# Optimization experiments

Hardware: AMD Instinct MI355X
Metric: run time of the kernel (lower is better)

Reference implementation:

```python
import jax, jax.numpy as jnp
import numpy as np

EPS = 1e-5

def binarize(x):
    # det Binarize: sign with zeros mapped to +1
    return jnp.where(x >= 0, 1.0, -1.0).astype(x.dtype)

def conv3x3(x, w, stride=1):
    return jax.lax.conv_general_dilated(
        x, w, window_strides=(stride, stride), padding=((1, 1), (1, 1)),
        dimension_numbers=('NCHW', 'OIHW', 'NCHW'))

def batchnorm_train(x, gamma, beta):
    # training-mode BN: biased batch stats over (N, H, W)
    mean = jnp.mean(x, axis=(0, 2, 3), keepdims=True)
    var = jnp.mean(jnp.square(x - mean), axis=(0, 2, 3), keepdims=True)
    xn = (x - mean) * jax.lax.rsqrt(var + EPS)
    return xn * gamma[None, :, None, None] + beta[None, :, None, None]

def setup_inputs() -> dict:
    key = jax.random.key(0)
    k1, k2, k3 = jax.random.split(key, 3)
    C = 256
    return {
        'x': jax.random.normal(k1, (64, C, 28, 28), dtype=jnp.float32),
        'w1': jax.random.normal(k2, (C, C, 3, 3), dtype=jnp.float32) * 0.05,
        'w2': jax.random.normal(k3, (C, C, 3, 3), dtype=jnp.float32) * 0.05,
        'gamma1': jnp.ones((C,), jnp.float32),
        'beta1': jnp.zeros((C,), jnp.float32),
        'gamma2': jnp.ones((C,), jnp.float32),
        'beta2': jnp.zeros((C,), jnp.float32),
    }

def reference(x, w1, w2, gamma1, beta1, gamma2, beta2):
    residual = x
    # conv1: binarized activations and weights, 3x3 pad=1 stride=1
    out = conv3x3(binarize(x), binarize(w1))
    out = batchnorm_train(out, gamma1, beta1)
    out = jnp.clip(out, -1.0, 1.0)  # Hardtanh
    # conv2
    out = conv3x3(binarize(out), binarize(w2))
    out = out + residual
    # do_bntan
    out = batchnorm_train(out, gamma2, beta2)
    out = jnp.clip(out, -1.0, 1.0)
    return out
```

## Files before the change

kernel.cpp:

```cpp
#include <hip/hip_runtime.h>
#include <stdint.h>

typedef int v4i __attribute__((ext_vector_type(4)));

constexpr int C     = 256;
constexpr int H     = 28, W = 28;
constexpr int HW    = H * W;
constexpr int NB    = 64;
constexpr int GP    = NB * HW;
constexpr int CNT   = GP;
constexpr int TOTAL = NB * C * HW;
constexpr int MT    = 112;
constexpr int NBLK  = GP / MT;
constexpr int LROWS = 176;
constexpr int ZROW  = LROWS * 16;
constexpr int GPB   = GP / 256;

__device__ __forceinline__ void pack_x_item(int local, int t, const float* __restrict__ x,
                                            v4i* __restrict__ xb, double* __restrict__ stats) {
    const int ch = local / GPB;
    const int gp = (local % GPB) * 256 + t;
    if (ch == 0 && gp < 1024) stats[gp] = 0.0;
    const int n = gp / HW, p = gp % HW;
    const float* base = x + (size_t)n * C * HW + p + (size_t)(ch * 16) * HW;
    int b0 = 0, b1 = 0, b2 = 0, b3 = 0;
#pragma unroll
    for (int e = 0; e < 16; ++e) {
        float v = base[(size_t)e * HW];
        int b = (v < 0.f) ? 0xFF : 0x01;
        int sh = (e & 3) * 8;
        if (e < 4) b0 |= b << sh; else if (e < 8) b1 |= b << sh;
        else if (e < 12) b2 |= b << sh; else b3 |= b << sh;
    }
    v4i o; o.x = b0; o.y = b1; o.z = b2; o.w = b3;
    xb[(size_t)ch * GP + gp] = o;
}

__device__ __forceinline__ void finalize_coefs(int t, const double* __restrict__ sum,
                                               const double* __restrict__ sumsq,
                                               const float* __restrict__ gamma,
                                               const float* __restrict__ beta,
                                               float* __restrict__ s_scale,
                                               float* __restrict__ s_shift) {
    double mean = sum[t] / (double)CNT;
    double var  = sumsq[t] / (double)CNT - mean * mean;
    double inv  = 1.0 / sqrt(var + 1e-5);
    s_scale[t] = (float)inv * gamma[t];
    s_shift[t] = beta[t] - (float)(mean * inv) * gamma[t];
}

__global__ void pack_all_kernel(const float* __restrict__ pw1, const float* __restrict__ pw2,
                                const float* __restrict__ x,
                                v4i* __restrict__ wbf1, v4i* __restrict__ wbf2,
                                v4i* __restrict__ xb, double* __restrict__ stats) {
    __shared__ signed char sgn[36864];
    const int t = threadIdx.x;
    const int bid = blockIdx.x;
    if (bid < 32) {
        const int g = bid & 15;
        const float* w = (bid >> 4) ? pw2 : pw1;
        v4i* dst       = (bid >> 4) ? wbf2 : wbf1;
        const float4* wg = (const float4*)(w + (size_t)g * 16 * 2304);
        int* sg4 = (int*)sgn;
        for (int pass = 0; pass < 36; ++pass) {
            const int m4 = pass * 256 + t;
            float4 v = wg[m4];
            int pk = (v.x < 0.f ? 0xFF : 0x01)
                   | ((v.y < 0.f ? 0xFF : 0x01) << 8)
                   | ((v.z < 0.f ? 0xFF : 0x01) << 16)
                   | ((v.w < 0.f ? 0xFF : 0x01) << 24);
            sg4[m4] = pk;
        }
        __syncthreads();
        const int l = t & 63, kb = t >> 6;
        const int colb = (l & 15) * 2304;
        const int cib  = kb * 64 + (l >> 4) * 16;
        for (int tp = 0; tp < 9; ++tp) {
            int b0 = 0, b1 = 0, b2 = 0, b3 = 0;
#pragma unroll
            for (int e = 0; e < 16; ++e) {
                int b = (int)(unsigned char)sgn[colb + (cib + e) * 9 + tp];
                int sh = (e & 3) * 8;
                if (e < 4) b0 |= b << sh; else if (e < 8) b1 |= b << sh;
                else if (e < 12) b2 |= b << sh; else b3 |= b << sh;
            }
            v4i o; o.x = b0; o.y = b1; o.z = b2; o.w = b3;
            dst[((tp * 4 + kb) * 16 + g) * 64 + l] = o;
        }
    } else {
        pack_x_item(bid - 32, t, x, xb, stats);
    }
}

__global__ void bn_signpack_kernel(const short* __restrict__ y,
                                   const double* __restrict__ sum,
                                   const double* __restrict__ sumsq,
                                   const float* __restrict__ gamma,
                                   const float* __restrict__ beta,
                                   v4i* __restrict__ xb) {
    __shared__ float s_scale[C], s_shift[C];
    const int t = threadIdx.x;
    finalize_coefs(t, sum, sumsq, gamma, beta, s_scale, s_shift);
    __syncthreads();
    const int local = blockIdx.x;
    const int ch = local / GPB;
    const int gp = (local % GPB) * 256 + t;
    const int n = gp / HW, p = gp % HW;
    const short* base = y + (size_t)n * C * HW + p + (size_t)(ch * 16) * HW;
    int b0 = 0, b1 = 0, b2 = 0, b3 = 0;
#pragma unroll
    for (int e = 0; e < 16; ++e) {
        const int c = ch * 16 + e;
        float z = (float)base[(size_t)e * HW] * s_scale[c] + s_shift[c];
        int b = (z < 0.f) ? 0xFF : 0x01;
        int sh = (e & 3) * 8;
        if (e < 4) b0 |= b << sh; else if (e < 8) b1 |= b << sh;
        else if (e < 12) b2 |= b << sh; else b3 |= b << sh;
    }
    v4i o; o.x = b0; o.y = b1; o.z = b2; o.w = b3;
    xb[(size_t)ch * GP + gp] = o;
}


#define ACCD(m) v4i c##m##_0={0,0,0,0}, c##m##_1={0,0,0,0}, \
                    c##m##_2={0,0,0,0}, c##m##_3={0,0,0,0};
#define ACC_DECL ACCD(0) ACCD(1) ACCD(2) ACCD(3) ACCD(4) ACCD(5) ACCD(6)

#define MFMA(a,b,c) c = __builtin_amdgcn_mfma_i32_16x16x64_i8(a, b, c, 0, 0, 0);

#define B_LOADQ(P, idx) { const v4i* bp = wbf + (idx); \
    P##0 = bp[0]; P##1 = bp[64]; P##2 = bp[128]; P##3 = bp[192]; }

#define ARD(P, m, cb) P##m = xl[R##m + ((cb) ^ S##m)];
#define ARDALL(P, cb) ARD(P,0,cb) ARD(P,1,cb) ARD(P,2,cb) ARD(P,3,cb) \
                      ARD(P,4,cb) ARD(P,5,cb) ARD(P,6,cb)

#define MFMAG(A,B,g) MFMA(A##0,B##g,c0_##g) MFMA(A##1,B##g,c1_##g) MFMA(A##2,B##g,c2_##g) \
                     MFMA(A##3,B##g,c3_##g) MFMA(A##4,B##g,c4_##g) MFMA(A##5,B##g,c5_##g) \
                     MFMA(A##6,B##g,c6_##g)
#define MFMA_C(A,B) __builtin_amdgcn_s_setprio(1); \
    MFMAG(A,B,0) MFMAG(A,B,1) MFMAG(A,B,2) MFMAG(A,B,3) \
    __builtin_amdgcn_s_setprio(0);

#define TV1(m) { const bool mk = ((unsigned)(cm##m + dc) < 28u) && \
                                 ((unsigned)(rm##m + dr) < 28u); \
    R##m = mk ? (lrb + 16 * (m)) * 16 : ZROW; S##m = mk ? sm : 0; }
#define TAPVARS(TPX) { const int dr = (TPX)/3 - 1, dc = (TPX)%3 - 1; \
    const int lrb = 32 + llo + dr * W + dc; const int sm = lrb & 15; \
    TV1(0) TV1(1) TV1(2) TV1(3) TV1(4) TV1(5) TV1(6) }

#define PMV(m) const int gx##m = gp0 + (m)*16 + llo; \
    const int pmv##m = gx##m % HW; \
    const int rm##m = pmv##m / W, cm##m = pmv##m % W;

#define EPIV(m,g) { \
    const int gpv = gp0 + (m)*16 + lhi*4; \
    const int nn = gpv / HW; const int pp = gpv - nn*HW; \
    const size_t base = (size_t)nn*(C*HW) + (size_t)(wn*64+(g)*16+llo)*HW + pp; \
    const v4i cc = c##m##_##g; \
    if constexpr (HAS_RES) { \
        const float4 r = *(const float4*)(residual + base); \
        float4 o; o.x = (float)cc.x + r.x; o.y = (float)cc.y + r.y; \
        o.z = (float)cc.z + r.z; o.w = (float)cc.w + r.w; \
        *(float4*)((float*)yout + base) = o; \
        sy##g += o.x + o.y + o.z + o.w; \
        sq##g += o.x*o.x + o.y*o.y + o.z*o.z + o.w*o.w; \
    } else { \
        int2 o; o.x = (cc.x & 0xFFFF) | (cc.y << 16); \
        o.y = (cc.z & 0xFFFF) | (cc.w << 16); \
        *(int2*)((short*)yout + base) = o; \
        const float fx = (float)cc.x, fy = (float)cc.y, fz = (float)cc.z, fw = (float)cc.w; \
        sy##g += fx + fy + fz + fw; \
        sq##g += fx*fx + fy*fy + fz*fz + fw*fw; \
    } }
#define EPIM(m) EPIV(m,0) EPIV(m,1) EPIV(m,2) EPIV(m,3)

#define REDN(g) { float s1 = sy##g, s2 = sq##g; \
    s1 += __shfl_down(s1, 32); s1 += __shfl_down(s1, 16); \
    s2 += __shfl_down(s2, 32); s2 += __shfl_down(s2, 16); \
    if (l < 16) { const int co = wn*64 + (g)*16 + l; \
        atomicAdd(&sum[co], (double)s1); atomicAdd(&sumsq[co], (double)s2); } }

template<bool HAS_RES, typename OUT_T>
__launch_bounds__(256, 2)
__global__ void bconv_mfma(const v4i* __restrict__ xb,
                           const v4i* __restrict__ wbf,
                           const float* __restrict__ residual,
                           OUT_T* __restrict__ yout,
                           double* __restrict__ sum, double* __restrict__ sumsq) {
    __shared__ v4i xl[LROWS * 16 + 16];
    const int t   = threadIdx.x;
    const int gp0 = blockIdx.x * MT;

    for (int pass = 0; pass < 11; ++pass) {
        const int i = pass * 256 + t;
        const int c = i / LROWS;
        const int r = i - c * LROWS;
        int gsrc = min(max(gp0 - 32 + r, 0), GP - 1);
        xl[r * 16 + (c ^ (r & 15))] = xb[(size_t)c * GP + gsrc];
    }
    if (t < 16) { v4i z = {0,0,0,0}; xl[ZROW + t] = z; }
    __syncthreads();

    const int l = t & 63, wn = t >> 6;
    const int llo = l & 15, lhi = l >> 4;

    PMV(0) PMV(1) PMV(2) PMV(3) PMV(4) PMV(5) PMV(6)

    ACC_DECL
    const int bw = wn * 256 + l;

    int R0,R1,R2,R3,R4,R5,R6, S0,S1,S2,S3,S4,S5,S6;
    TAPVARS(0)
    v4i bP0,bP1,bP2,bP3, bQ0,bQ1,bQ2,bQ3;
    v4i aP0,aP1,aP2,aP3,aP4,aP5,aP6, aQ0,aQ1,aQ2,aQ3,aQ4,aQ5,aQ6;
    B_LOADQ(bP, bw)
    ARDALL(aP, lhi)

#pragma unroll 1
    for (int tp = 0; tp < 9; ++tp) {
        const int tb = bw + tp * 4096;
        B_LOADQ(bQ, tb + 1024)
        ARDALL(aQ, 4 + lhi)
        MFMA_C(aP, bP)
        B_LOADQ(bP, tb + 2048)
        ARDALL(aP, 8 + lhi)
        MFMA_C(aQ, bQ)
        B_LOADQ(bQ, tb + 3072)
        ARDALL(aQ, 12 + lhi)
        MFMA_C(aP, bP)
        const int tpn = (tp < 8) ? tp + 1 : 8;
        TAPVARS(tpn)
        B_LOADQ(bP, bw + tpn * 4096)
        ARDALL(aP, lhi)
        MFMA_C(aQ, bQ)
    }

    float sy0 = 0, sy1 = 0, sy2 = 0, sy3 = 0;
    float sq0 = 0, sq1 = 0, sq2 = 0, sq3 = 0;
    EPIM(0) EPIM(1) EPIM(2) EPIM(3) EPIM(4) EPIM(5) EPIM(6)
    REDN(0) REDN(1) REDN(2) REDN(3)
}

__global__ void bn_clip_kernel(const float4* __restrict__ z,
                               const double* __restrict__ sum,
                               const double* __restrict__ sumsq,
                               const float* __restrict__ gamma,
                               const float* __restrict__ beta,
                               float4* __restrict__ out) {
    __shared__ float s_scale[C], s_shift[C];
    const int t = threadIdx.x;
    finalize_coefs(t, sum, sumsq, gamma, beta, s_scale, s_shift);
    __syncthreads();
    for (int i = blockIdx.x * blockDim.x + t; i < TOTAL / 4;
         i += gridDim.x * blockDim.x) {
        int c = (i / (HW / 4)) & (C - 1);
        float s = s_scale[c], b = s_shift[c];
        float4 v = z[i];
        v.x = fminf(1.f, fmaxf(-1.f, v.x * s + b));
        v.y = fminf(1.f, fmaxf(-1.f, v.y * s + b));
        v.z = fminf(1.f, fmaxf(-1.f, v.z * s + b));
        v.w = fminf(1.f, fmaxf(-1.f, v.w * s + b));
        out[i] = v;
    }
}

extern "C" void kernel_launch(void* const* d_in, const int* in_sizes, int n_in,
                              void* d_out, int out_size, void* d_ws, size_t ws_size,
                              hipStream_t stream) {
    const float* x  = (const float*)d_in[0];
    const float* w1 = (const float*)d_in[1];
    const float* w2 = (const float*)d_in[2];
    const float* g1 = (const float*)d_in[3];
    const float* b1 = (const float*)d_in[4];
    const float* g2 = (const float*)d_in[5];
    const float* b2 = (const float*)d_in[6];
    float* out = (float*)d_out;

    char* ws = (char*)d_ws;
    size_t off = 0;
    float* z2 = (float*)(ws + off);   off += (size_t)TOTAL * 4;
    v4i* xb1  = (v4i*)(ws + off);     off += (size_t)GP * 16 * 16;
    v4i* xb2  = (v4i*)(ws + off);     off += (size_t)GP * 16 * 16;
    v4i* wbf1 = (v4i*)(ws + off);     off += (size_t)36864 * 16;
    v4i* wbf2 = (v4i*)(ws + off);     off += (size_t)36864 * 16;
    double* stats = (double*)(ws + off); off += 4 * 256 * 8;
    double* sum1 = stats, *sumsq1 = stats + 256, *sum2 = stats + 512, *sumsq2 = stats + 768;

    short* y1 = (short*)d_out;

    pack_all_kernel<<<32 + 16 * GPB, 256, 0, stream>>>(w1, w2, x, wbf1, wbf2, xb1, stats);

    bconv_mfma<false, short><<<NBLK, 256, 0, stream>>>(xb1, wbf1, nullptr, y1, sum1, sumsq1);
    bn_signpack_kernel<<<16 * GPB, 256, 0, stream>>>(y1, sum1, sumsq1, g1, b1, xb2);
    bconv_mfma<true, float><<<NBLK, 256, 0, stream>>>(xb2, wbf2, x, z2, sum2, sumsq2);
    bn_clip_kernel<<<4096, 256, 0, stream>>>((const float4*)z2, sum2, sumsq2, g2, b2,
                                             (float4*)out);
}
```

Measured before the change: 203.1 us.

## Vectorize sign-pack kernels to four pixels per thread and hoist BN finalize

The x sign-pack and BN sign-pack kernels now have each thread handle four consecutive pixels with float4/short4 loads and write four packed vectors, so grids shrink fourfold. BN coefficient computation moves out of every block into a single-block finalize kernel that writes scale/shift buffers, which the sign-pack and clip kernels then just load. This cuts redundant double-precision work per block and widens global loads, at the cost of two extra kernel launches.

```diff
diff --git a/kernel.cpp b/kernel.cpp
--- a/kernel.cpp
+++ b/kernel.cpp
@@ -14,40 +14,14 @@
 constexpr int NBLK  = GP / MT;
 constexpr int LROWS = 176;
 constexpr int ZROW  = LROWS * 16;
-constexpr int GPB   = GP / 256;
-
-__device__ __forceinline__ void pack_x_item(int local, int t, const float* __restrict__ x,
-                                            v4i* __restrict__ xb, double* __restrict__ stats) {
-    const int ch = local / GPB;
-    const int gp = (local % GPB) * 256 + t;
-    if (ch == 0 && gp < 1024) stats[gp] = 0.0;
-    const int n = gp / HW, p = gp % HW;
-    const float* base = x + (size_t)n * C * HW + p + (size_t)(ch * 16) * HW;
-    int b0 = 0, b1 = 0, b2 = 0, b3 = 0;
-#pragma unroll
-    for (int e = 0; e < 16; ++e) {
-        float v = base[(size_t)e * HW];
-        int b = (v < 0.f) ? 0xFF : 0x01;
-        int sh = (e & 3) * 8;
-        if (e < 4) b0 |= b << sh; else if (e < 8) b1 |= b << sh;
-        else if (e < 12) b2 |= b << sh; else b3 |= b << sh;
-    }
-    v4i o; o.x = b0; o.y = b1; o.z = b2; o.w = b3;
-    xb[(size_t)ch * GP + gp] = o;
-}
-
-__device__ __forceinline__ void finalize_coefs(int t, const double* __restrict__ sum,
-                                               const double* __restrict__ sumsq,
-                                               const float* __restrict__ gamma,
-                                               const float* __restrict__ beta,
-                                               float* __restrict__ s_scale,
-                                               float* __restrict__ s_shift) {
-    double mean = sum[t] / (double)CNT;
-    double var  = sumsq[t] / (double)CNT - mean * mean;
-    double inv  = 1.0 / sqrt(var + 1e-5);
-    s_scale[t] = (float)inv * gamma[t];
-    s_shift[t] = beta[t] - (float)(mean * inv) * gamma[t];
-}
+
+
+#define SB(f) ((f) < 0.f ? 0xFF : 0x01)
+
+#define XPE(e, pw0, pw1, pw2, pw3, sh) { \
+    const float4 v = *(const float4*)(base + (size_t)(e) * HW); \
+    pw0 |= SB(v.x) << (sh); pw1 |= SB(v.y) << (sh); \
+    pw2 |= SB(v.z) << (sh); pw3 |= SB(v.w) << (sh); }
 
 __global__ void pack_all_kernel(const float* __restrict__ pw1, const float* __restrict__ pw2,
                                 const float* __restrict__ x,
@@ -65,10 +39,7 @@
         for (int pass = 0; pass < 36; ++pass) {
             const int m4 = pass * 256 + t;
             float4 v = wg[m4];
-            int pk = (v.x < 0.f ? 0xFF : 0x01)
-                   | ((v.y < 0.f ? 0xFF : 0x01) << 8)
-                   | ((v.z < 0.f ? 0xFF : 0x01) << 16)
-                   | ((v.w < 0.f ? 0xFF : 0x01) << 24);
+            int pk = SB(v.x) | (SB(v.y) << 8) | (SB(v.z) << 16) | (SB(v.w) << 24);
             sg4[m4] = pk;
         }
         __syncthreads();
@@ -88,37 +59,79 @@
             dst[((tp * 4 + kb) * 16 + g) * 64 + l] = o;
         }
     } else {
-        pack_x_item(bid - 32, t, x, xb, stats);
+        const int local = bid - 32;
+        const int ch = local / 49;
+        const int i4 = (local % 49) * 256 + t;
+        if (ch == 0 && i4 < 1024) stats[i4] = 0.0;
+        const int gp = i4 * 4;
+        const int n = gp / HW, p = gp % HW;
+        const float* base = x + (size_t)n * C * HW + (size_t)(ch * 16) * HW + p;
+        int a0=0,a1=0,a2=0,a3=0;
+        int b0=0,b1=0,b2=0,b3=0;
+        int c0=0,c1=0,c2=0,c3=0;
+        int d0=0,d1=0,d2=0,d3=0;
+        XPE( 0,a0,b0,c0,d0, 0) XPE( 1,a0,b0,c0,d0, 8) XPE( 2,a0,b0,c0,d0,16) XPE( 3,a0,b0,c0,d0,24)
+        XPE( 4,a1,b1,c1,d1, 0) XPE( 5,a1,b1,c1,d1, 8) XPE( 6,a1,b1,c1,d1,16) XPE( 7,a1,b1,c1,d1,24)
+        XPE( 8,a2,b2,c2,d2, 0) XPE( 9,a2,b2,c2,d2, 8) XPE(10,a2,b2,c2,d2,16) XPE(11,a2,b2,c2,d2,24)
+        XPE(12,a3,b3,c3,d3, 0) XPE(13,a3,b3,c3,d3, 8) XPE(14,a3,b3,c3,d3,16) XPE(15,a3,b3,c3,d3,24)
+        v4i* dst = xb + (size_t)ch * GP + gp;
+        v4i o0; o0.x=a0; o0.y=a1; o0.z=a2; o0.w=a3; dst[0] = o0;
+        v4i o1; o1.x=b0; o1.y=b1; o1.z=b2; o1.w=b3; dst[1] = o1;
+        v4i o2; o2.x=c0; o2.y=c1; o2.z=c2; o2.w=c3; dst[2] = o2;
+        v4i o3; o3.x=d0; o3.y=d1; o3.z=d2; o3.w=d3; dst[3] = o3;
     }
 }
 
+__global__ void finalize_kernel(const double* __restrict__ sum,
+                                const double* __restrict__ sumsq,
+                                const float* __restrict__ gamma,
+                                const float* __restrict__ beta,
+                                float* __restrict__ scale,
+                                float* __restrict__ shift) {
+    int c = threadIdx.x;
+    double mean = sum[c] / (double)CNT;
+    double var  = sumsq[c] / (double)CNT - mean * mean;
+    double inv  = 1.0 / sqrt(var + 1e-5);
+    scale[c] = (float)inv * gamma[c];
+    shift[c] = beta[c] - (float)(mean * inv) * gamma[c];
+}
+
+typedef short short4v __attribute__((ext_vector_type(4)));
+
+#define SPE(e, pw0, pw1, pw2, pw3, sh) { \
+    const short4v v = *(const short4v*)(base + (size_t)(e) * HW); \
+    const float sc = s_scale[chb + (e)], sf = s_shift[chb + (e)]; \
+    pw0 |= SB((float)v.x * sc + sf) << (sh); pw1 |= SB((float)v.y * sc + sf) << (sh); \
+    pw2 |= SB((float)v.z * sc + sf) << (sh); pw3 |= SB((float)v.w * sc + sf) << (sh); }
+
 __global__ void bn_signpack_kernel(const short* __restrict__ y,
-                                   const double* __restrict__ sum,
-                                   const double* __restrict__ sumsq,
-                                   const float* __restrict__ gamma,
-                                   const float* __restrict__ beta,
+                                   const float* __restrict__ scale,
+                                   const float* __restrict__ shift,
                                    v4i* __restrict__ xb) {
     __shared__ float s_scale[C], s_shift[C];
     const int t = threadIdx.x;
-    finalize_coefs(t, sum, sumsq, gamma, beta, s_scale, s_shift);
+    s_scale[t] = scale[t]; s_shift[t] = shift[t];
     __syncthreads();
     const int local = blockIdx.x;
-    const int ch = local / GPB;
-    const int gp = (local % GPB) * 256 + t;
+    const int ch = local / 49;
+    const int i4 = (local % 49) * 256 + t;
+    const int gp = i4 * 4;
     const int n = gp / HW, p = gp % HW;
-    const short* base = y + (size_t)n * C * HW + p + (size_t)(ch * 16) * HW;
-    int b0 = 0, b1 = 0, b2 = 0, b3 = 0;
-#pragma unroll
-    for (int e = 0; e < 16; ++e) {
-        const int c = ch * 16 + e;
-        float z = (float)base[(size_t)e * HW] * s_scale[c] + s_shift[c];
-        int b = (z < 0.f) ? 0xFF : 0x01;
-        int sh = (e & 3) * 8;
-        if (e < 4) b0 |= b << sh; else if (e < 8) b1 |= b << sh;
-        else if (e < 12) b2 |= b << sh; else b3 |= b << sh;
-    }
-    v4i o; o.x = b0; o.y = b1; o.z = b2; o.w = b3;
-    xb[(size_t)ch * GP + gp] = o;
+    const short* base = y + (size_t)n * C * HW + (size_t)(ch * 16) * HW + p;
+    const int chb = ch * 16;
+    int a0=0,a1=0,a2=0,a3=0;
+    int b0=0,b1=0,b2=0,b3=0;
+    int c0=0,c1=0,c2=0,c3=0;
+    int d0=0,d1=0,d2=0,d3=0;
+    SPE( 0,a0,b0,c0,d0, 0) SPE( 1,a0,b0,c0,d0, 8) SPE( 2,a0,b0,c0,d0,16) SPE( 3,a0,b0,c0,d0,24)
+    SPE( 4,a1,b1,c1,d1, 0) SPE( 5,a1,b1,c1,d1, 8) SPE( 6,a1,b1,c1,d1,16) SPE( 7,a1,b1,c1,d1,24)
+    SPE( 8,a2,b2,c2,d2, 0) SPE( 9,a2,b2,c2,d2, 8) SPE(10,a2,b2,c2,d2,16) SPE(11,a2,b2,c2,d2,24)
+    SPE(12,a3,b3,c3,d3, 0) SPE(13,a3,b3,c3,d3, 8) SPE(14,a3,b3,c3,d3,16) SPE(15,a3,b3,c3,d3,24)
+    v4i* dst = xb + (size_t)ch * GP + gp;
+    v4i o0; o0.x=a0; o0.y=a1; o0.z=a2; o0.w=a3; dst[0] = o0;
+    v4i o1; o1.x=b0; o1.y=b1; o1.z=b2; o1.w=b3; dst[1] = o1;
+    v4i o2; o2.x=c0; o2.y=c1; o2.z=c2; o2.w=c3; dst[2] = o2;
+    v4i o3; o3.x=d0; o3.y=d1; o3.z=d2; o3.w=d3; dst[3] = o3;
 }
 
 
@@ -243,14 +256,12 @@
 }
 
 __global__ void bn_clip_kernel(const float4* __restrict__ z,
-                               const double* __restrict__ sum,
-                               const double* __restrict__ sumsq,
-                               const float* __restrict__ gamma,
-                               const float* __restrict__ beta,
+                               const float* __restrict__ scale,
+                               const float* __restrict__ shift,
                                float4* __restrict__ out) {
     __shared__ float s_scale[C], s_shift[C];
     const int t = threadIdx.x;
-    finalize_coefs(t, sum, sumsq, gamma, beta, s_scale, s_shift);
+    s_scale[t] = scale[t]; s_shift[t] = shift[t];
     __syncthreads();
     for (int i = blockIdx.x * blockDim.x + t; i < TOTAL / 4;
          i += gridDim.x * blockDim.x) {
@@ -286,14 +297,17 @@
     v4i* wbf2 = (v4i*)(ws + off);     off += (size_t)36864 * 16;
     double* stats = (double*)(ws + off); off += 4 * 256 * 8;
     double* sum1 = stats, *sumsq1 = stats + 256, *sum2 = stats + 512, *sumsq2 = stats + 768;
+    float* coefs = (float*)(ws + off);   off += 4 * 256 * 4;
+    float* scale1 = coefs, *shift1 = coefs + 256, *scale2 = coefs + 512, *shift2 = coefs + 768;
 
     short* y1 = (short*)d_out;
 
-    pack_all_kernel<<<32 + 16 * GPB, 256, 0, stream>>>(w1, w2, x, wbf1, wbf2, xb1, stats);
+    pack_all_kernel<<<32 + 784, 256, 0, stream>>>(w1, w2, x, wbf1, wbf2, xb1, stats);
 
     bconv_mfma<false, short><<<NBLK, 256, 0, stream>>>(xb1, wbf1, nullptr, y1, sum1, sumsq1);
-    bn_signpack_kernel<<<16 * GPB, 256, 0, stream>>>(y1, sum1, sumsq1, g1, b1, xb2);
+    finalize_kernel<<<1, 256, 0, stream>>>(sum1, sumsq1, g1, b1, scale1, shift1);
+    bn_signpack_kernel<<<784, 256, 0, stream>>>(y1, scale1, shift1, xb2);
     bconv_mfma<true, float><<<NBLK, 256, 0, stream>>>(xb2, wbf2, x, z2, sum2, sumsq2);
-    bn_clip_kernel<<<4096, 256, 0, stream>>>((const float4*)z2, sum2, sumsq2, g2, b2,
-                                             (float4*)out);
-}
+    finalize_kernel<<<1, 256, 0, stream>>>(sum2, sumsq2, g2, b2, scale2, shift2);
+    bn_clip_kernel<<<4096, 256, 0, stream>>>((const float4*)z2, scale2, shift2, (float4*)out);
+}
```

Result: slower. 215.5 us (+6.1%).
